# Kernel optimization log

Hardware: AMD Instinct MI355X
Metric: run time of the kernel (lower is better)

Reference implementation:

```python
import jax, jax.numpy as jnp
import numpy as np

B, N, DIM = 4, 1024, 768
HEADS, DIM_HEAD = 12, 64
INNER = HEADS * DIM_HEAD  # 768
SCALE = DIM ** -0.5


def setup_inputs() -> dict:
    key = jax.random.key(0)
    ks = jax.random.split(key, 5)
    return {
        "x": jax.random.normal(ks[0], (B, N, DIM), dtype=jnp.float32),
        "pos_embedding": jax.random.normal(ks[1], (B, N, DIM), dtype=jnp.float32),
        "w_qkv": jax.random.normal(ks[2], (DIM, 3 * INNER), dtype=jnp.float32) * (DIM ** -0.5),
        "w_qk_pos": jax.random.normal(ks[3], (DIM, 2 * INNER), dtype=jnp.float32) * (DIM ** -0.5),
        "w_out": jax.random.normal(ks[4], (INNER, DIM), dtype=jnp.float32) * (INNER ** -0.5),
        "b_out": jnp.zeros((DIM,), dtype=jnp.float32),
    }


def _split_heads(t):
    # [b, n, h*d] -> [b, h, n, d]
    b, n, _ = t.shape
    return t.reshape(b, n, HEADS, DIM_HEAD).transpose(0, 2, 1, 3)


def reference(x, pos_embedding, w_qkv, w_qk_pos, w_out, b_out):
    qkv = x @ w_qkv  # [b, n, 3*inner]
    q, k, v = (_split_heads(t) for t in jnp.split(qkv, 3, axis=-1))
    qk_pos = pos_embedding @ w_qk_pos  # [b, n, 2*inner]
    q_pos, k_pos = (_split_heads(t) for t in jnp.split(qk_pos, 2, axis=-1))

    dots = jnp.einsum('bhid,bhjd->bhij', q, k) * SCALE
    dots_pos = jnp.einsum('bhid,bhjd->bhij', q_pos, k_pos) * SCALE
    dots = (dots + dots_pos) * 0.5  # averaged content+positional scores

    attn = jax.nn.softmax(dots, axis=-1)
    out = jnp.einsum('bhij,bhjd->bhid', attn, v)
    out = out.transpose(0, 2, 1, 3).reshape(x.shape[0], x.shape[1], INNER)
    return out @ w_out + b_out
```

## Files before the change

### kernel.cpp

```cpp
#include <hip/hip_runtime.h>
#include <cstdint>
#include <cstddef>

typedef __bf16 bf16;
typedef __bf16 bf16x8 __attribute__((ext_vector_type(8)));
typedef __bf16 bf16x4v __attribute__((ext_vector_type(4)));
typedef float  f32x4  __attribute__((ext_vector_type(4)));

#define MFMA(a, b, c) __builtin_amdgcn_mfma_f32_16x16x32_bf16((a), (b), (c), 0, 0, 0)

typedef __attribute__((address_space(3))) unsigned int  lds_u32;
typedef __attribute__((address_space(1))) unsigned int glob_u32;


__global__ void k_cvt2(const float* __restrict__ x, const float* __restrict__ pos,
                       bf16* __restrict__ xb, bf16* __restrict__ posb) {
    int i = blockIdx.x * 256 + threadIdx.x;
    const float* in = x; bf16* out = xb;
    if (i >= 786432) { i -= 786432; in = pos; out = posb; }
    float4 v = reinterpret_cast<const float4*>(in)[i];
    bf16x4v o; o[0] = (bf16)v.x; o[1] = (bf16)v.y; o[2] = (bf16)v.z; o[3] = (bf16)v.w;
    reinterpret_cast<bf16x4v*>(out)[i] = o;
}

__global__ void k_tr(const float* __restrict__ w_qkv, const float* __restrict__ w_qk_pos,
                     const float* __restrict__ w_out,
                     bf16* __restrict__ wqkvT, bf16* __restrict__ wqkposT,
                     bf16* __restrict__ woutT) {
    __shared__ float t[32][33];
    int bx = blockIdx.x;
    const float* in; bf16* out; int N;
    if (bx < 72)       { in = w_qkv;    out = wqkvT;   N = 2304; }
    else if (bx < 120) { in = w_qk_pos; out = wqkposT; N = 1536; bx -= 72; }
    else               { in = w_out;    out = woutT;   N = 768;  bx -= 120; }
    const int n0 = bx * 32, k0 = blockIdx.y * 32;
    const int tx = threadIdx.x & 31, ty = threadIdx.x >> 5;
#pragma unroll
    for (int r = 0; r < 32; r += 8)
        t[ty + r][tx] = in[(size_t)(k0 + ty + r) * N + n0 + tx];
    __syncthreads();
#pragma unroll
    for (int r = 0; r < 32; r += 8)
        out[(size_t)(n0 + ty + r) * 768 + k0 + tx] = (bf16)t[tx][ty + r];
}

__launch_bounds__(256, 3)
__global__ void k_gemm12(const bf16* __restrict__ xb, const bf16* __restrict__ posb,
                         const bf16* __restrict__ wqkvT, const bf16* __restrict__ wqkposT,
                         bf16* __restrict__ qcat, bf16* __restrict__ kcat,
                         bf16* __restrict__ vT) {
    __shared__ bf16 lA[2][128][32];

    const int tid  = threadIdx.x;
    const int lane = tid & 63, wave = tid >> 6;
    const int quad = lane >> 4, col = lane & 15;
    const int sw2  = (col >> 1) & 3;
    const int wm = (wave >> 1) * 64, wn = (wave & 1) * 64;

    const int fid = blockIdx.x;
    const int xcd = fid & 7, s = fid >> 3;
    const int sx = s % 15, sy = s / 15;
    int bx = (xcd & 1) * 15 + sx;
    const int by = (xcd >> 1) * 8 + sy;

    int mode, nBase;
    const bf16 *A, *BT;
    if (bx < 18) { mode = 0; A = xb;   BT = wqkvT;   nBase = bx * 128; }
    else         { mode = 1; A = posb; BT = wqkposT; nBase = (bx - 18) * 128; }
    const int mBase = by * 128;

    const bf16* Ap = A  + (size_t)mBase * 768;
    const bf16* Bp = BT + (size_t)nBase * 768;

#define STAGE_A(buf, k0)                                                        \
    _Pragma("unroll")                                                           \
    for (int j = 0; j < 2; ++j) {                                               \
        int idx = (wave * 2 + j) * 64 + lane;                                   \
        int row = idx >> 2, c = (idx & 3) ^ ((row >> 1) & 3);                   \
        __builtin_amdgcn_global_load_lds(                                       \
            (const glob_u32*)(Ap + (size_t)row * 768 + (k0) + c * 8),           \
            (lds_u32*)((char*)&lA[buf][0][0] + (wave * 2 + j) * 1024), 16, 0, 0);\
    }

    const bf16* Bq[4];
#pragma unroll
    for (int ni = 0; ni < 4; ++ni)
        Bq[ni] = Bp + (size_t)(wn + ni * 16 + col) * 768 + quad * 8;

    bf16x8 bcur[4], bnxt[4];
#pragma unroll
    for (int ni = 0; ni < 4; ++ni) bcur[ni] = *(const bf16x8*)(Bq[ni]);

    f32x4 acc[4][4];
#pragma unroll
    for (int mi = 0; mi < 4; ++mi)
#pragma unroll
        for (int ni = 0; ni < 4; ++ni) acc[mi][ni] = f32x4{0.f, 0.f, 0.f, 0.f};

    STAGE_A(0, 0)
#pragma unroll
    for (int it = 0; it < 24; ++it) {
        const int cur = it & 1, nxt = cur ^ 1;
        __syncthreads();
        if (it < 23) {
            STAGE_A(nxt, (it + 1) * 32)
#pragma unroll
            for (int ni = 0; ni < 4; ++ni)
                bnxt[ni] = *(const bf16x8*)(Bq[ni] + (it + 1) * 32);
        }
        bf16x8 af[4];
#pragma unroll
        for (int mi = 0; mi < 4; ++mi)
            af[mi] = *(const bf16x8*)&lA[cur][wm + mi * 16 + col][(quad ^ sw2) * 8];
#pragma unroll
        for (int mi = 0; mi < 4; ++mi)
#pragma unroll
            for (int ni = 0; ni < 4; ++ni)
                acc[mi][ni] = MFMA(af[mi], bcur[ni], acc[mi][ni]);
#pragma unroll
        for (int ni = 0; ni < 4; ++ni) bcur[ni] = bnxt[ni];
    }
#undef STAGE_A

    const float c2s = 0.018042195912f * 1.44269504089f;
    const int bb = mBase >> 10;
    const int sr0 = (mBase & 1023) + wm + quad * 4;
#pragma unroll
    for (int ni = 0; ni < 4; ++ni) {
        const int nb = nBase + wn + ni * 16;
        const int which = (mode == 0) ? (nb >= 1536 ? 2 : (nb >= 768 ? 1 : 0))
                                      : (nb >= 768 ? 1 : 0);
        const int rem = nb - which * 768;
        const int hh = rem >> 6, dd0 = rem & 63;
        const size_t hb = (size_t)(bb * 12 + hh);
        if (mode == 0 && which == 2) {
            bf16* dstv = vT + (hb * 64 + dd0 + col) * 1024 + sr0;
#pragma unroll
            for (int mi = 0; mi < 4; ++mi) {
                bf16x4v pk;
#pragma unroll
                for (int r = 0; r < 4; ++r) pk[r] = (bf16)acc[mi][ni][r];
                *(bf16x4v*)(dstv + mi * 16) = pk;
            }
        } else {
            const float scl = (which == 0) ? c2s : 1.0f;
            bf16* dstq = (which == 0 ? qcat : kcat)
                       + (hb * 1024 + sr0) * 128 + (mode == 1 ? 64 : 0) + dd0 + col;
#pragma unroll
            for (int mi = 0; mi < 4; ++mi)
#pragma unroll
                for (int r = 0; r < 4; ++r)
                    dstq[(size_t)(mi * 16 + r) * 128] = (bf16)(acc[mi][ni][r] * scl);
        }
    }
}

__launch_bounds__(256, 3)
__global__ void k_attn(const bf16* __restrict__ qcat, const bf16* __restrict__ kcat,
                       const bf16* __restrict__ vT, bf16* __restrict__ attn_out) {
    __shared__ bf16 lK[2][64][128];
    __shared__ bf16 lV[2][64][64];

    const int tid  = threadIdx.x;
    const int lane = tid & 63, wave = tid >> 6;
    const int quad = lane >> 4, col = lane & 15;
    const int sw   = col & 7;
    const int q01  = quad >> 1, qlo = quad & 1;

    const int fid = blockIdx.x;
    const int xcd = fid & 7, s = fid >> 3;
    const int qt = s & 15;
    const int unit = (s >> 4) * 8 + xcd;
    const int b = unit / 12, h = unit % 12;

    const bf16* Qb = qcat + (size_t)unit * 1024 * 128;
    const bf16* Kb = kcat + (size_t)unit * 1024 * 128;
    const bf16* Vb = vT   + (size_t)unit * 64 * 1024;

    const int kidx = wave * 256 + lane;
    const int vidx = wave * 128 + lane;

#define STAGE_K(buf, kv0)                                                      \
    _Pragma("unroll")                                                          \
    for (int j = 0; j < 4; ++j) {                                              \
        int idx = kidx + j * 64;                                               \
        int row = idx >> 4, c = idx & 15, csrc = c ^ (row & 7);                \
        __builtin_amdgcn_global_load_lds(                                      \
            (const glob_u32*)(Kb + (size_t)((kv0) + row) * 128 + csrc * 8),    \
            (lds_u32*)(&lK[buf][0][0] + (wave * 4 + j) * 512), 16, 0, 0);      \
    }
#define STAGE_V(buf, kv0)                                                      \
    _Pragma("unroll")                                                          \
    for (int j = 0; j < 2; ++j) {                                              \
        int idx = vidx + j * 64;                                               \
        int row = idx >> 3, c = idx & 7, csrc = c ^ (row & 7);                 \
        __builtin_amdgcn_global_load_lds(                                      \
            (const glob_u32*)(Vb + (size_t)row * 1024 + (kv0) + csrc * 8),     \
            (lds_u32*)(&lV[buf][0][0] + (wave * 2 + j) * 512), 16, 0, 0);      \
    }

    bf16x8 qb[4];
    {
        const bf16* qrow = Qb + (size_t)(qt * 64 + wave * 16 + col) * 128;
#pragma unroll
        for (int f = 0; f < 4; ++f) qb[f] = *(const bf16x8*)(qrow + f * 32 + quad * 8);
    }

    f32x4 o[4];
#pragma unroll
    for (int vt = 0; vt < 4; ++vt) o[vt] = f32x4{0.f, 0.f, 0.f, 0.f};
    float lsum = 0.f;

    STAGE_K(0, 0)
    STAGE_V(0, 0)

    for (int it = 0; it < 16; ++it) {
        const int cur = it & 1, nxt = cur ^ 1;
        __syncthreads();
        if (it < 15) {
            const int kv1 = (it + 1) * 64;
            STAGE_K(nxt, kv1)
            STAGE_V(nxt, kv1)
        }

        f32x4 st[4];
#pragma unroll
        for (int t = 0; t < 4; ++t) st[t] = f32x4{0.f, 0.f, 0.f, 0.f};
#pragma unroll
        for (int t = 0; t < 4; ++t)
#pragma unroll
            for (int f = 0; f < 4; ++f) {
                bf16x8 kf = *(const bf16x8*)&lK[cur][t * 16 + col][((f * 4 + quad) ^ sw) * 8];
                st[t] = MFMA(kf, qb[f], st[t]);
            }

        bf16x8 pbf[2];
#pragma unroll
        for (int c = 0; c < 2; ++c) {
#pragma unroll
            for (int r = 0; r < 4; ++r) {
                float p0 = exp2f(st[2 * c][r]);
                float p1 = exp2f(st[2 * c + 1][r]);
                lsum += p0 + p1;
                pbf[c][r]     = (bf16)p0;
                pbf[c][4 + r] = (bf16)p1;
            }
        }

#pragma unroll
        for (int c = 0; c < 2; ++c)
#pragma unroll
            for (int vt = 0; vt < 4; ++vt) {
                const bf16* vrow = &lV[cur][vt * 16 + col][0];
                bf16x4v va = *(const bf16x4v*)(vrow + ((c * 4 + q01) ^ sw) * 8 + qlo * 4);
                bf16x4v vb = *(const bf16x4v*)(vrow + ((c * 4 + 2 + q01) ^ sw) * 8 + qlo * 4);
                bf16x8 vf;
#pragma unroll
                for (int i = 0; i < 4; ++i) { vf[i] = va[i]; vf[4 + i] = vb[i]; }
                o[vt] = MFMA(vf, pbf[c], o[vt]);
            }
    }

    float l = lsum;
    l += __shfl_xor(l, 16, 64);
    l += __shfl_xor(l, 32, 64);
    const float inv = 1.f / l;

    const int qrow = qt * 64 + wave * 16 + col;
    bf16* dst = attn_out + ((size_t)b * 1024 + qrow) * 768 + h * 64;
#pragma unroll
    for (int vt = 0; vt < 4; ++vt)
#pragma unroll
        for (int r = 0; r < 4; ++r)
            dst[vt * 16 + quad * 4 + r] = (bf16)(o[vt][r] * inv);
#undef STAGE_K
#undef STAGE_V
}

__launch_bounds__(256, 3)
__global__ void k_gemm_out(const bf16* __restrict__ aout, const bf16* __restrict__ woutT,
                           const float* __restrict__ bias, float* __restrict__ out) {
    __shared__ bf16 lA[2][128][32];
    __shared__ bf16 lB[2][64][32];

    const int tid  = threadIdx.x;
    const int lane = tid & 63, wave = tid >> 6;
    const int quad = lane >> 4, col = lane & 15;
    const int sw2  = (col >> 1) & 3;
    const int wm = (wave >> 1) * 64, wn = (wave & 1) * 32;

    const int fid = blockIdx.x;
    const int xcd = fid & 7, s = fid >> 3;
    const int sx = s % 6, sy = s / 6;
    const int bx = (xcd & 1) * 6 + sx;
    const int by = (xcd >> 1) * 8 + sy;

    const int mBase = by * 128, nBase = bx * 64;

    const bf16* Ap = aout  + (size_t)mBase * 768;
    const bf16* Bp = woutT + (size_t)nBase * 768;

#define STAGE_O(buf, k0)                                                        \
    _Pragma("unroll")                                                           \
    for (int j = 0; j < 2; ++j) {                                               \
        int idx = (wave * 2 + j) * 64 + lane;                                   \
        int row = idx >> 2, c = (idx & 3) ^ ((row >> 1) & 3);                   \
        __builtin_amdgcn_global_load_lds(                                       \
            (const glob_u32*)(Ap + (size_t)row * 768 + (k0) + c * 8),           \
            (lds_u32*)((char*)&lA[buf][0][0] + (wave * 2 + j) * 1024), 16, 0, 0);\
    }                                                                           \
    {                                                                           \
        int idx = wave * 64 + lane;                                             \
        int row = idx >> 2, c = (idx & 3) ^ ((row >> 1) & 3);                   \
        __builtin_amdgcn_global_load_lds(                                       \
            (const glob_u32*)(Bp + (size_t)row * 768 + (k0) + c * 8),           \
            (lds_u32*)((char*)&lB[buf][0][0] + wave * 1024), 16, 0, 0);         \
    }

    f32x4 acc[4][2];
#pragma unroll
    for (int mi = 0; mi < 4; ++mi)
#pragma unroll
        for (int ni = 0; ni < 2; ++ni) acc[mi][ni] = f32x4{0.f, 0.f, 0.f, 0.f};

    STAGE_O(0, 0)
    for (int it = 0; it < 24; ++it) {
        const int cur = it & 1, nxt = cur ^ 1;
        __syncthreads();
        if (it < 23) STAGE_O(nxt, (it + 1) * 32)

        bf16x8 af[4], bfg[2];
#pragma unroll
        for (int mi = 0; mi < 4; ++mi)
            af[mi]  = *(const bf16x8*)&lA[cur][wm + mi * 16 + col][(quad ^ sw2) * 8];
#pragma unroll
        for (int ni = 0; ni < 2; ++ni)
            bfg[ni] = *(const bf16x8*)&lB[cur][wn + ni * 16 + col][(quad ^ sw2) * 8];
#pragma unroll
        for (int mi = 0; mi < 4; ++mi)
#pragma unroll
            for (int ni = 0; ni < 2; ++ni)
                acc[mi][ni] = MFMA(af[mi], bfg[ni], acc[mi][ni]);
    }
#undef STAGE_O

#pragma unroll
    for (int mi = 0; mi < 4; ++mi)
#pragma unroll
        for (int ni = 0; ni < 2; ++ni)
#pragma unroll
            for (int r = 0; r < 4; ++r) {
                int m = mBase + wm + mi * 16 + quad * 4 + r;
                int n = nBase + wn + ni * 16 + col;
                out[(size_t)m * 768 + n] = acc[mi][ni][r] + bias[n];
            }
}

extern "C" void kernel_launch(void* const* d_in, const int* in_sizes, int n_in,
                              void* d_out, int out_size, void* d_ws, size_t ws_size,
                              hipStream_t stream) {
    const float* x        = (const float*)d_in[0];
    const float* pos      = (const float*)d_in[1];
    const float* w_qkv    = (const float*)d_in[2];
    const float* w_qk_pos = (const float*)d_in[3];
    const float* w_out    = (const float*)d_in[4];
    const float* b_out    = (const float*)d_in[5];
    float* out = (float*)d_out;

    char* ws = (char*)d_ws;
    bf16* xb      = (bf16*)(ws);
    bf16* posb    = (bf16*)(ws + 6291456);
    bf16* wqkvT   = (bf16*)(ws + 12582912);
    bf16* wqkposT = (bf16*)(ws + 16121856);
    bf16* woutT   = (bf16*)(ws + 18481152);
    bf16* qcat    = (bf16*)(ws + 19660800);
    bf16* kcat    = (bf16*)(ws + 32243712);
    bf16* vT      = (bf16*)(ws + 44826624);
    bf16* aout    = (bf16*)(ws + 51118080);

    k_cvt2<<<6144, 256, 0, stream>>>(x, pos, xb, posb);
    k_tr<<<dim3(144, 24), 256, 0, stream>>>(w_qkv, w_qk_pos, w_out, wqkvT, wqkposT, woutT);
    k_gemm12<<<960, 256, 0, stream>>>(xb, posb, wqkvT, wqkposT, qcat, kcat, vT);
    k_attn<<<768, 256, 0, stream>>>(qcat, kcat, vT, aout);
    k_gemm_out<<<384, 256, 0, stream>>>(aout, woutT, b_out, out);
}
```

Before: 201.5 us.

## Merge prep kernels and stage GEMM B tiles through LDS via async loads

Fuses the bf16 conversion and weight-transpose kernels into a single launch, removing one kernel boundary. In the QKV/pos projection GEMM, B-operand fragments are now loaded into a double-buffered, swizzled LDS tile with global_load_lds instead of direct per-lane global register loads. The goal is more coalesced B traffic overlapped with compute. In exchange, LDS use per block doubles (which may limit occupancy), adds LDS read traffic, and the K loop is no longer fully unrolled.

```diff
diff --git a/kernel.cpp b/kernel.cpp
--- a/kernel.cpp
+++ b/kernel.cpp
@@ -13,27 +13,29 @@
 typedef __attribute__((address_space(1))) unsigned int glob_u32;
 
 
-__global__ void k_cvt2(const float* __restrict__ x, const float* __restrict__ pos,
-                       bf16* __restrict__ xb, bf16* __restrict__ posb) {
-    int i = blockIdx.x * 256 + threadIdx.x;
-    const float* in = x; bf16* out = xb;
-    if (i >= 786432) { i -= 786432; in = pos; out = posb; }
-    float4 v = reinterpret_cast<const float4*>(in)[i];
-    bf16x4v o; o[0] = (bf16)v.x; o[1] = (bf16)v.y; o[2] = (bf16)v.z; o[3] = (bf16)v.w;
-    reinterpret_cast<bf16x4v*>(out)[i] = o;
-}
-
-__global__ void k_tr(const float* __restrict__ w_qkv, const float* __restrict__ w_qk_pos,
-                     const float* __restrict__ w_out,
-                     bf16* __restrict__ wqkvT, bf16* __restrict__ wqkposT,
-                     bf16* __restrict__ woutT) {
+__global__ void k_prep(const float* __restrict__ x, const float* __restrict__ pos,
+                       const float* __restrict__ w_qkv, const float* __restrict__ w_qk_pos,
+                       const float* __restrict__ w_out,
+                       bf16* __restrict__ xb, bf16* __restrict__ posb,
+                       bf16* __restrict__ wqkvT, bf16* __restrict__ wqkposT,
+                       bf16* __restrict__ woutT) {
     __shared__ float t[32][33];
-    int bx = blockIdx.x;
+    const int blk = blockIdx.x;
+    if (blk < 6144) {
+        int i = blk * 256 + threadIdx.x;
+        const float* in = x; bf16* out = xb;
+        if (i >= 786432) { i -= 786432; in = pos; out = posb; }
+        float4 v = reinterpret_cast<const float4*>(in)[i];
+        bf16x4v o; o[0] = (bf16)v.x; o[1] = (bf16)v.y; o[2] = (bf16)v.z; o[3] = (bf16)v.w;
+        reinterpret_cast<bf16x4v*>(out)[i] = o;
+        return;
+    }
+    int bx = (blk - 6144) % 144, ky = (blk - 6144) / 144;
     const float* in; bf16* out; int N;
     if (bx < 72)       { in = w_qkv;    out = wqkvT;   N = 2304; }
     else if (bx < 120) { in = w_qk_pos; out = wqkposT; N = 1536; bx -= 72; }
     else               { in = w_out;    out = woutT;   N = 768;  bx -= 120; }
-    const int n0 = bx * 32, k0 = blockIdx.y * 32;
+    const int n0 = bx * 32, k0 = ky * 32;
     const int tx = threadIdx.x & 31, ty = threadIdx.x >> 5;
 #pragma unroll
     for (int r = 0; r < 32; r += 8)
@@ -50,6 +52,7 @@
                          bf16* __restrict__ qcat, bf16* __restrict__ kcat,
                          bf16* __restrict__ vT) {
     __shared__ bf16 lA[2][128][32];
+    __shared__ bf16 lB[2][128][32];
 
     const int tid  = threadIdx.x;
     const int lane = tid & 63, wave = tid >> 6;
@@ -72,7 +75,7 @@
     const bf16* Ap = A  + (size_t)mBase * 768;
     const bf16* Bp = BT + (size_t)nBase * 768;
 
-#define STAGE_A(buf, k0)                                                        \
+#define STAGE12(buf, k0)                                                        \
     _Pragma("unroll")                                                           \
     for (int j = 0; j < 2; ++j) {                                               \
         int idx = (wave * 2 + j) * 64 + lane;                                   \
@@ -80,16 +83,10 @@
         __builtin_amdgcn_global_load_lds(                                       \
             (const glob_u32*)(Ap + (size_t)row * 768 + (k0) + c * 8),           \
             (lds_u32*)((char*)&lA[buf][0][0] + (wave * 2 + j) * 1024), 16, 0, 0);\
-    }
-
-    const bf16* Bq[4];
-#pragma unroll
-    for (int ni = 0; ni < 4; ++ni)
-        Bq[ni] = Bp + (size_t)(wn + ni * 16 + col) * 768 + quad * 8;
-
-    bf16x8 bcur[4], bnxt[4];
-#pragma unroll
-    for (int ni = 0; ni < 4; ++ni) bcur[ni] = *(const bf16x8*)(Bq[ni]);
+        __builtin_amdgcn_global_load_lds(                                       \
+            (const glob_u32*)(Bp + (size_t)row * 768 + (k0) + c * 8),           \
+            (lds_u32*)((char*)&lB[buf][0][0] + (wave * 2 + j) * 1024), 16, 0, 0);\
+    }
 
     f32x4 acc[4][4];
 #pragma unroll
@@ -97,30 +94,26 @@
 #pragma unroll
         for (int ni = 0; ni < 4; ++ni) acc[mi][ni] = f32x4{0.f, 0.f, 0.f, 0.f};
 
-    STAGE_A(0, 0)
-#pragma unroll
+    STAGE12(0, 0)
     for (int it = 0; it < 24; ++it) {
         const int cur = it & 1, nxt = cur ^ 1;
         __syncthreads();
-        if (it < 23) {
-            STAGE_A(nxt, (it + 1) * 32)
+        if (it < 23) STAGE12(nxt, (it + 1) * 32)
+
+        bf16x8 af[4], bfg[4];
+#pragma unroll
+        for (int mi = 0; mi < 4; ++mi)
+            af[mi]  = *(const bf16x8*)&lA[cur][wm + mi * 16 + col][(quad ^ sw2) * 8];
+#pragma unroll
+        for (int ni = 0; ni < 4; ++ni)
+            bfg[ni] = *(const bf16x8*)&lB[cur][wn + ni * 16 + col][(quad ^ sw2) * 8];
+#pragma unroll
+        for (int mi = 0; mi < 4; ++mi)
 #pragma unroll
             for (int ni = 0; ni < 4; ++ni)
-                bnxt[ni] = *(const bf16x8*)(Bq[ni] + (it + 1) * 32);
-        }
-        bf16x8 af[4];
-#pragma unroll
-        for (int mi = 0; mi < 4; ++mi)
-            af[mi] = *(const bf16x8*)&lA[cur][wm + mi * 16 + col][(quad ^ sw2) * 8];
-#pragma unroll
-        for (int mi = 0; mi < 4; ++mi)
-#pragma unroll
-            for (int ni = 0; ni < 4; ++ni)
-                acc[mi][ni] = MFMA(af[mi], bcur[ni], acc[mi][ni]);
-#pragma unroll
-        for (int ni = 0; ni < 4; ++ni) bcur[ni] = bnxt[ni];
-    }
-#undef STAGE_A
+                acc[mi][ni] = MFMA(af[mi], bfg[ni], acc[mi][ni]);
+    }
+#undef STAGE12
 
     const float c2s = 0.018042195912f * 1.44269504089f;
     const int bb = mBase >> 10;
@@ -378,8 +371,8 @@
     bf16* vT      = (bf16*)(ws + 44826624);
     bf16* aout    = (bf16*)(ws + 51118080);
 
-    k_cvt2<<<6144, 256, 0, stream>>>(x, pos, xb, posb);
-    k_tr<<<dim3(144, 24), 256, 0, stream>>>(w_qkv, w_qk_pos, w_out, wqkvT, wqkposT, woutT);
+    k_prep<<<9600, 256, 0, stream>>>(x, pos, w_qkv, w_qk_pos, w_out,
+                                     xb, posb, wqkvT, wqkposT, woutT);
     k_gemm12<<<960, 256, 0, stream>>>(xb, posb, wqkvT, wqkposT, qcat, kcat, vT);
     k_attn<<<768, 256, 0, stream>>>(qcat, kcat, vT, aout);
     k_gemm_out<<<384, 256, 0, stream>>>(aout, woutT, b_out, out);
```

Measured after the change: 178.6 us. 11.4% less time.
